# Kernel tuning notes

Measured on AMD Instinct MI355X. Metric: run time of the kernel, lower is better.

Reference implementation:

```python
import jax, jax.numpy as jnp
import numpy as np
from itertools import combinations

NUM_ENT = 7
DIM_ENT = 256
REL_HIDDEN = 256
HIDDEN = 1024
BATCH = 16384
PAIRS = np.array(list(combinations(range(NUM_ENT), 2)), dtype=np.int32)  # [21, 2]


def setup_inputs() -> dict:
    key = jax.random.key(0)
    k1, k2, k3 = jax.random.split(key, 3)
    ctx = jax.random.normal(k1, (BATCH, NUM_ENT * DIM_ENT), dtype=jnp.float32)
    # torch init: uniform(-init_range, init_range) weights, zero bias
    W_rel = jax.random.uniform(k2, (2 * DIM_ENT, REL_HIDDEN), dtype=jnp.float32, minval=-0.01, maxval=0.01)
    b_rel = jnp.zeros((REL_HIDDEN,), dtype=jnp.float32)
    W_fc = jax.random.uniform(k3, (NUM_ENT * DIM_ENT + REL_HIDDEN, HIDDEN), dtype=jnp.float32, minval=-0.01, maxval=0.01)
    b_fc = jnp.zeros((HIDDEN,), dtype=jnp.float32)
    return {"ctx": ctx, "W_rel": W_rel, "b_rel": b_rel, "W_fc": W_fc, "b_fc": b_fc}


def reference(ctx, W_rel, b_rel, W_fc, b_fc):
    B = ctx.shape[0]
    ents = ctx.reshape(B, NUM_ENT, DIM_ENT)
    idx_i = jnp.asarray(PAIRS[:, 0])
    idx_j = jnp.asarray(PAIRS[:, 1])
    # gather both endpoints of each of the 21 pairs: [B, 21, 2*DIM_ENT]
    pair_feat = jnp.concatenate([ents[:, idx_i, :], ents[:, idx_j, :]], axis=-1)
    # batched small Linear + Tanh: [B, 21, REL_HIDDEN]
    rel = jnp.tanh(jnp.einsum("bpe,eh->bph", pair_feat, W_rel) + b_rel)
    # faithful replication of torch: cat pair-major then view(B, rel_hidden, -1).sum(2)
    rel = rel.reshape(B, 21 * REL_HIDDEN).reshape(B, REL_HIDDEN, 21).sum(axis=2)
    inpt = jnp.concatenate([ctx, rel], axis=1)  # [B, input_size]
    # dropout output is discarded in the original forward (no-op); fc1 uses inpt
    out = jnp.tanh(inpt @ W_fc + b_fc)
    return out[None, :, :]  # [1, B, HIDDEN]
```

## Files before the change

kernel.cpp:

```cpp
#include <hip/hip_runtime.h>

typedef unsigned short u16;
typedef unsigned int u32;
typedef __attribute__((ext_vector_type(8))) short short8;
typedef __attribute__((ext_vector_type(4))) float f32x4;
typedef __attribute__((ext_vector_type(2))) u32 u32x2;
typedef const __attribute__((address_space(1))) unsigned int g_u32;
typedef __attribute__((address_space(3))) unsigned int l_u32;

#define BATCH 16384
#define XCOLS 2048

__device__ __forceinline__ void gload16(const void* g, void* l) {
  __builtin_amdgcn_global_load_lds((g_u32*)g, (l_u32*)l, 16, 0, 0);
}
__device__ __forceinline__ u16 f2bf(float f) {
  u32 x = __builtin_bit_cast(u32, f);
  x += 0x7fffu + ((x >> 16) & 1u);
  return (u16)(x >> 16);
}
__device__ __forceinline__ int swz(int P) { return P ^ (((P >> 7) & 7) << 4); }

__device__ __forceinline__ float fast_tanh(float x) {
  float e = __builtin_amdgcn_exp2f(x * 2.885390081777927f);
  return __builtin_fmaf(-2.0f, __builtin_amdgcn_rcpf(e + 1.0f), 1.0f);
}

#define PIPK 0544333222211111000000ULL
#define PJPK 0665654654365432654321ULL

__global__ void prep_ctx(const float* __restrict__ ctx, u16* __restrict__ X) {
  const int total = BATCH * 224;
  for (int u = blockIdx.x * blockDim.x + threadIdx.x; u < total;
       u += gridDim.x * blockDim.x) {
    int b = u / 224, c8 = u - b * 224;
    const float4* s = (const float4*)(ctx + (size_t)b * 1792 + c8 * 8);
    float4 v0 = s[0], v1 = s[1];
    short8 o;
    o[0] = (short)f2bf(v0.x); o[1] = (short)f2bf(v0.y);
    o[2] = (short)f2bf(v0.z); o[3] = (short)f2bf(v0.w);
    o[4] = (short)f2bf(v1.x); o[5] = (short)f2bf(v1.y);
    o[6] = (short)f2bf(v1.z); o[7] = (short)f2bf(v1.w);
    *(short8*)(X + (size_t)b * XCOLS + c8 * 8) = o;
  }
}

__global__ void prep_wrel(const float* __restrict__ Wr, u16* __restrict__ WcT) {
  int idx = blockIdx.x * 256 + threadIdx.x;
  if (idx >= 512 * 256) return;
  int n = idx >> 8, k = idx & 255;
  float v = (n < 256) ? Wr[k * 256 + n] : Wr[(256 + k) * 256 + (n - 256)];
  WcT[idx] = f2bf(v);
}

__global__ void prep_wfc(const float* __restrict__ W, u16* __restrict__ WT) {
  __shared__ float t[64][65];
  int k0 = blockIdx.x * 64;
  int n0 = blockIdx.y * 64;
  int tx = threadIdx.x & 63, ty = threadIdx.x >> 6;
  #pragma unroll
  for (int i = 0; i < 64; i += 4)
    t[ty + i][tx] = W[(size_t)(k0 + ty + i) * 1024 + n0 + tx];
  __syncthreads();
  #pragma unroll
  for (int i = 0; i < 64; i += 4) {
    int n = ty + i;
    WT[(size_t)(n0 + n) * XCOLS + k0 + tx] = f2bf(t[tx][n]);
  }
}

__global__ __launch_bounds__(512, 4) void gemm1_fused(u16* __restrict__ X, const u16* __restrict__ WcT,
                                                      const float* __restrict__ b_rel) {
  __shared__ __align__(16) u16 smem[36864];
  char* sb = (char*)smem;
  const int tid = threadIdx.x;
  const int wid = tid >> 6, lane = tid & 63;
  const int b_base = blockIdx.x * 8;
  f32x4 bias[4] = {};
  if (wid < 4) {
    #pragma unroll
    for (int n = 0; n < 4; ++n)
      bias[n] = *(const f32x4*)(b_rel + wid * 64 + n * 16 + ((lane >> 4) << 2));
  }
  f32x4 acc[4][4] = {};
  for (int kt = 0; kt < 4; ++kt) {
    const int kb = kt * 64;
    {
      int L = swz(tid * 16);
      int row = L >> 7, koff = (L & 127) >> 1;
      int r = row < 56 ? row : 55;
      int bl = r / 7, e = r - bl * 7;
      gload16(X + (size_t)(b_base + bl) * XCOLS + e * 256 + kb + koff, sb + wid * 1024);
    }
    #pragma unroll
    for (int i = 0; i < 8; ++i) {
      int slot = i * 512 + tid;
      int L = swz(slot * 16);
      int rn = L >> 7, koff = (L & 127) >> 1;
      gload16(WcT + rn * 256 + kb + koff, sb + 8192 + (i * 512 + wid * 64) * 16);
    }
    __syncthreads();
    #pragma unroll
    for (int kk = 0; kk < 64; kk += 32) {
      short8 a[4], b[4];
      #pragma unroll
      for (int m = 0; m < 4; ++m) {
        int row = m * 16 + (lane & 15);
        int L = row * 128 + kk * 2 + ((lane >> 4) << 4);
        a[m] = *(const short8*)(sb + swz(L));
      }
      #pragma unroll
      for (int n = 0; n < 4; ++n) {
        int rn = wid * 64 + n * 16 + (lane & 15);
        int L = rn * 128 + kk * 2 + ((lane >> 4) << 4);
        b[n] = *(const short8*)(sb + 8192 + swz(L));
      }
      #pragma unroll
      for (int m = 0; m < 4; ++m)
        #pragma unroll
        for (int n = 0; n < 4; ++n)
          acc[m][n] = __builtin_amdgcn_mfma_f32_16x16x32_bf16(b[n], a[m], acc[m][n], 0, 0, 0);
    }
    __syncthreads();
  }
  float* Tbuf = (float*)(sb + 28672);
  auto stage = [&](int rd) {
    #pragma unroll
    for (int m = 0; m < 4; ++m) {
      int row = m * 16 + (lane & 15);
      int lr = row - rd * 14;
      if (lr >= 0 && lr < 14) {
        #pragma unroll
        for (int n = 0; n < 4; ++n) {
          f32x4 val = acc[m][n] + bias[n];
          int h0 = wid * 64 + n * 16 + ((lane >> 4) << 2);
          int L = lr * 2048 + h0 * 4;
          *(f32x4*)(sb + (L ^ ((lr & 7) << 4))) = val;
        }
      }
    }
  };
  stage(0);
  __syncthreads();
  for (int rd = 0; rd < 4; ++rd) {
    for (int i = tid; i < 2688; i += 512) {
      int bb = i >= 1344;
      int k4 = (i - bb * 1344) << 2;
      int p = k4 >> 8, h0 = k4 & 255;
      int li = bb * 7 + (int)((PIPK >> (3 * p)) & 7);
      int lj = bb * 7 + (int)((PJPK >> (3 * p)) & 7);
      int Lu = (li * 2048 + h0 * 4) ^ ((li & 7) << 4);
      int Lv = (lj * 2048 + 1024 + h0 * 4) ^ ((lj & 7) << 4);
      f32x4 uu = *(const f32x4*)(sb + Lu);
      f32x4 vv = *(const f32x4*)(sb + Lv);
      f32x4 t;
      t[0] = fast_tanh(uu[0] + vv[0]);
      t[1] = fast_tanh(uu[1] + vv[1]);
      t[2] = fast_tanh(uu[2] + vv[2]);
      t[3] = fast_tanh(uu[3] + vv[3]);
      *(f32x4*)(sb + 28672 + (bb * 5376 + k4) * 4) = t;
    }
    __syncthreads();
    {
      int bb = tid >> 8, r = tid & 255;
      const float* T = Tbuf + bb * 5376 + r * 21;
      float s = 0.f;
      #pragma unroll
      for (int c = 0; c < 21; ++c) s += T[c];
      X[(size_t)(b_base + rd * 2 + bb) * XCOLS + 1792 + r] = f2bf(s);
    }
    if (rd < 3) stage(rd + 1);
    __syncthreads();
  }
}

__global__ __launch_bounds__(256, 3) void gemm2(const u16* __restrict__ X, const u16* __restrict__ WT,
                                                const float* __restrict__ b_fc, float* __restrict__ out) {
  __shared__ __align__(16) u16 smem[16384];
  char* sb = (char*)smem;
  const int tid = threadIdx.x;
  const int wid = tid >> 6, lane = tid & 63;
  const int wr = wid >> 1, wc = wid & 1;
  int bid = blockIdx.x;
  int sw = (bid & 7) * 128 + (bid >> 3);
  int bm = sw >> 3, bn = sw & 7;
  const size_t mBase = (size_t)bm * 128;
  const int nBase = bn * 128;
  f32x4 acc[4][4] = {};
  for (int kt = 0; kt < 32; ++kt) {
    const int kb = kt * 64;
    #pragma unroll
    for (int i = 0; i < 4; ++i) {
      int cb = (wid + i * 4) * 64;
      int L = swz((cb + lane) * 16);
      int row = L >> 7, koff = (L & 127) >> 1;
      gload16(X + (mBase + row) * XCOLS + kb + koff, sb + cb * 16);
      gload16(WT + (size_t)(nBase + row) * XCOLS + kb + koff, sb + 16384 + cb * 16);
    }
    __syncthreads();
    #pragma unroll
    for (int kk = 0; kk < 64; kk += 32) {
      short8 a[4], b[4];
      #pragma unroll
      for (int m = 0; m < 4; ++m) {
        int row = wr * 64 + m * 16 + (lane & 15);
        int L = row * 128 + kk * 2 + ((lane >> 4) << 4);
        a[m] = *(const short8*)(sb + swz(L));
      }
      #pragma unroll
      for (int n = 0; n < 4; ++n) {
        int rn = wc * 64 + n * 16 + (lane & 15);
        int L = rn * 128 + kk * 2 + ((lane >> 4) << 4);
        b[n] = *(const short8*)(sb + 16384 + swz(L));
      }
      #pragma unroll
      for (int m = 0; m < 4; ++m)
        #pragma unroll
        for (int n = 0; n < 4; ++n)
          acc[m][n] = __builtin_amdgcn_mfma_f32_16x16x32_bf16(a[m], b[n], acc[m][n], 0, 0, 0);
    }
    __syncthreads();
  }
  #pragma unroll
  for (int m = 0; m < 4; ++m) {
    int row0 = wr * 64 + m * 16 + ((lane >> 4) << 2);
    #pragma unroll
    for (int n = 0; n < 4; ++n) {
      int col = nBase + wc * 64 + n * 16 + (lane & 15);
      float bias = b_fc[col];
      #pragma unroll
      for (int v = 0; v < 4; ++v)
        out[(mBase + row0 + v) * 1024 + col] = fast_tanh(acc[m][n][v] + bias);
    }
  }
}

extern "C" void kernel_launch(void* const* d_in, const int* in_sizes, int n_in,
                              void* d_out, int out_size, void* d_ws, size_t ws_size,
                              hipStream_t stream) {
  const float* ctx   = (const float*)d_in[0];
  const float* W_rel = (const float*)d_in[1];
  const float* b_rel = (const float*)d_in[2];
  const float* W_fc  = (const float*)d_in[3];
  const float* b_fc  = (const float*)d_in[4];
  float* out = (float*)d_out;
  u16* X    = (u16*)d_ws;
  u16* WcT  = X + (size_t)BATCH * XCOLS;
  u16* WfcT = WcT + 512 * 256;
  prep_ctx<<<2048, 256, 0, stream>>>(ctx, X);
  prep_wrel<<<512, 256, 0, stream>>>(W_rel, WcT);
  prep_wfc<<<dim3(32, 16), 256, 0, stream>>>(W_fc, WfcT);
  gemm1_fused<<<2048, 512, 0, stream>>>(X, WcT, b_rel);
  gemm2<<<1024, 256, 0, stream>>>(X, WfcT, b_fc, out);
}
```

Baseline: 201.7 us.

## Triple-buffer gemm2 with 256x128 tiles and fuse pair-tanh reduction in gemm1

```diff
diff --git a/kernel.cpp b/kernel.cpp
--- a/kernel.cpp
+++ b/kernel.cpp
@@ -4,7 +4,6 @@
 typedef unsigned int u32;
 typedef __attribute__((ext_vector_type(8))) short short8;
 typedef __attribute__((ext_vector_type(4))) float f32x4;
-typedef __attribute__((ext_vector_type(2))) u32 u32x2;
 typedef const __attribute__((address_space(1))) unsigned int g_u32;
 typedef __attribute__((address_space(3))) unsigned int l_u32;
 
@@ -123,7 +122,6 @@
     }
     __syncthreads();
   }
-  float* Tbuf = (float*)(sb + 28672);
   auto stage = [&](int rd) {
     #pragma unroll
     for (int m = 0; m < 4; ++m) {
@@ -133,100 +131,130 @@
         #pragma unroll
         for (int n = 0; n < 4; ++n) {
           f32x4 val = acc[m][n] + bias[n];
-          int h0 = wid * 64 + n * 16 + ((lane >> 4) << 2);
-          int L = lr * 2048 + h0 * 4;
+          int h0c = wid * 64 + n * 16 + ((lane >> 4) << 2);
+          int L = lr * 2048 + h0c * 4;
           *(f32x4*)(sb + (L ^ ((lr & 7) << 4))) = val;
         }
       }
     }
   };
   stage(0);
+  const int bb = tid >> 8;
+  const int r = tid & 255;
+  const int R21 = r * 21;
+  const int p0 = R21 >> 8;
+  const int h0 = R21 & 255;
+  const int cx = 256 - h0;
+  const int p1 = p0 < 20 ? p0 + 1 : 20;
+  const int li0 = bb * 7 + (int)((PIPK >> (3 * p0)) & 7);
+  const int lj0 = bb * 7 + (int)((PJPK >> (3 * p0)) & 7);
+  const int li1 = bb * 7 + (int)((PIPK >> (3 * p1)) & 7);
+  const int lj1 = bb * 7 + (int)((PJPK >> (3 * p1)) & 7);
+  const int bU0 = li0 * 2048 + h0 * 4, sU0 = (li0 & 7) << 4;
+  const int bV0 = lj0 * 2048 + 1024 + h0 * 4, sV0 = (lj0 & 7) << 4;
+  const int bU1 = li1 * 2048 - cx * 4, sU1 = (li1 & 7) << 4;
+  const int bV1 = lj1 * 2048 + 1024 - cx * 4, sV1 = (lj1 & 7) << 4;
   __syncthreads();
   for (int rd = 0; rd < 4; ++rd) {
-    for (int i = tid; i < 2688; i += 512) {
-      int bb = i >= 1344;
-      int k4 = (i - bb * 1344) << 2;
-      int p = k4 >> 8, h0 = k4 & 255;
-      int li = bb * 7 + (int)((PIPK >> (3 * p)) & 7);
-      int lj = bb * 7 + (int)((PJPK >> (3 * p)) & 7);
-      int Lu = (li * 2048 + h0 * 4) ^ ((li & 7) << 4);
-      int Lv = (lj * 2048 + 1024 + h0 * 4) ^ ((lj & 7) << 4);
-      f32x4 uu = *(const f32x4*)(sb + Lu);
-      f32x4 vv = *(const f32x4*)(sb + Lv);
-      f32x4 t;
-      t[0] = fast_tanh(uu[0] + vv[0]);
-      t[1] = fast_tanh(uu[1] + vv[1]);
-      t[2] = fast_tanh(uu[2] + vv[2]);
-      t[3] = fast_tanh(uu[3] + vv[3]);
-      *(f32x4*)(sb + 28672 + (bb * 5376 + k4) * 4) = t;
-    }
+    float s = 0.f;
+    #pragma unroll
+    for (int c = 0; c < 21; ++c) {
+      bool sg = c >= cx;
+      int aU = ((sg ? bU1 : bU0) + 4 * c) ^ (sg ? sU1 : sU0);
+      int aV = ((sg ? bV1 : bV0) + 4 * c) ^ (sg ? sV1 : sV0);
+      float u = *(const float*)(sb + aU);
+      float v = *(const float*)(sb + aV);
+      s += fast_tanh(u + v);
+    }
+    X[(size_t)(b_base + rd * 2 + bb) * XCOLS + 1792 + r] = f2bf(s);
     __syncthreads();
-    {
-      int bb = tid >> 8, r = tid & 255;
-      const float* T = Tbuf + bb * 5376 + r * 21;
-      float s = 0.f;
-      #pragma unroll
-      for (int c = 0; c < 21; ++c) s += T[c];
-      X[(size_t)(b_base + rd * 2 + bb) * XCOLS + 1792 + r] = f2bf(s);
-    }
-    if (rd < 3) stage(rd + 1);
-    __syncthreads();
-  }
-}
-
-__global__ __launch_bounds__(256, 3) void gemm2(const u16* __restrict__ X, const u16* __restrict__ WT,
+    if (rd < 3) {
+      stage(rd + 1);
+      __syncthreads();
+    }
+  }
+}
+
+#define G2_BUF 49152
+__global__ __launch_bounds__(512, 2) void gemm2(const u16* __restrict__ X, const u16* __restrict__ WT,
                                                 const float* __restrict__ b_fc, float* __restrict__ out) {
-  __shared__ __align__(16) u16 smem[16384];
+  __shared__ __align__(16) u16 smem[73728];
   char* sb = (char*)smem;
   const int tid = threadIdx.x;
   const int wid = tid >> 6, lane = tid & 63;
-  const int wr = wid >> 1, wc = wid & 1;
+  const int wr = wid >> 2, wc = wid & 3;
   int bid = blockIdx.x;
-  int sw = (bid & 7) * 128 + (bid >> 3);
+  int sw = (bid & 7) * 64 + (bid >> 3);
   int bm = sw >> 3, bn = sw & 7;
-  const size_t mBase = (size_t)bm * 128;
+  const size_t mBase = (size_t)bm * 256;
   const int nBase = bn * 128;
-  f32x4 acc[4][4] = {};
-  for (int kt = 0; kt < 32; ++kt) {
-    const int kb = kt * 64;
+  f32x4 acc[8][2] = {};
+  auto stage2 = [&](int t, int q) {
+    char* Ab = sb + q * G2_BUF;
+    char* Bb = Ab + 32768;
+    const int kb = t * 64;
     #pragma unroll
     for (int i = 0; i < 4; ++i) {
-      int cb = (wid + i * 4) * 64;
-      int L = swz((cb + lane) * 16);
+      int L = swz((i * 512 + tid) * 16);
       int row = L >> 7, koff = (L & 127) >> 1;
-      gload16(X + (mBase + row) * XCOLS + kb + koff, sb + cb * 16);
-      gload16(WT + (size_t)(nBase + row) * XCOLS + kb + koff, sb + 16384 + cb * 16);
-    }
-    __syncthreads();
+      gload16(X + (mBase + row) * XCOLS + kb + koff, Ab + (i * 512 + wid * 64) * 16);
+    }
+    #pragma unroll
+    for (int i = 0; i < 2; ++i) {
+      int L = swz((i * 512 + tid) * 16);
+      int row = L >> 7, koff = (L & 127) >> 1;
+      gload16(WT + (size_t)(nBase + row) * XCOLS + kb + koff, Bb + (i * 512 + wid * 64) * 16);
+    }
+  };
+  auto compute = [&](int q) {
+    char* Ab = sb + q * G2_BUF;
+    char* Bb = Ab + 32768;
     #pragma unroll
     for (int kk = 0; kk < 64; kk += 32) {
-      short8 a[4], b[4];
-      #pragma unroll
-      for (int m = 0; m < 4; ++m) {
-        int row = wr * 64 + m * 16 + (lane & 15);
+      short8 a[8], b[2];
+      #pragma unroll
+      for (int m = 0; m < 8; ++m) {
+        int row = wr * 128 + m * 16 + (lane & 15);
         int L = row * 128 + kk * 2 + ((lane >> 4) << 4);
-        a[m] = *(const short8*)(sb + swz(L));
-      }
-      #pragma unroll
-      for (int n = 0; n < 4; ++n) {
-        int rn = wc * 64 + n * 16 + (lane & 15);
+        a[m] = *(const short8*)(Ab + swz(L));
+      }
+      #pragma unroll
+      for (int n = 0; n < 2; ++n) {
+        int rn = wc * 32 + n * 16 + (lane & 15);
         int L = rn * 128 + kk * 2 + ((lane >> 4) << 4);
-        b[n] = *(const short8*)(sb + 16384 + swz(L));
-      }
-      #pragma unroll
-      for (int m = 0; m < 4; ++m)
+        b[n] = *(const short8*)(Bb + swz(L));
+      }
+      __builtin_amdgcn_s_setprio(1);
+      #pragma unroll
+      for (int m = 0; m < 8; ++m)
         #pragma unroll
-        for (int n = 0; n < 4; ++n)
+        for (int n = 0; n < 2; ++n)
           acc[m][n] = __builtin_amdgcn_mfma_f32_16x16x32_bf16(a[m], b[n], acc[m][n], 0, 0, 0);
-    }
-    __syncthreads();
-  }
+      __builtin_amdgcn_s_setprio(0);
+    }
+  };
+  stage2(0, 0);
+  stage2(1, 1);
+  int qc = 0;
+  for (int t = 0; t < 31; ++t) {
+    asm volatile("s_waitcnt vmcnt(6)" ::: "memory");
+    __builtin_amdgcn_s_barrier();
+    if (t < 30) {
+      int qs = qc + 2 >= 3 ? qc - 1 : qc + 2;
+      stage2(t + 2, qs);
+    }
+    compute(qc);
+    qc = qc + 1 >= 3 ? 0 : qc + 1;
+  }
+  asm volatile("s_waitcnt vmcnt(0)" ::: "memory");
+  __builtin_amdgcn_s_barrier();
+  compute(qc);
   #pragma unroll
-  for (int m = 0; m < 4; ++m) {
-    int row0 = wr * 64 + m * 16 + ((lane >> 4) << 2);
-    #pragma unroll
-    for (int n = 0; n < 4; ++n) {
-      int col = nBase + wc * 64 + n * 16 + (lane & 15);
+  for (int m = 0; m < 8; ++m) {
+    int row0 = wr * 128 + m * 16 + ((lane >> 4) << 2);
+    #pragma unroll
+    for (int n = 0; n < 2; ++n) {
+      int col = nBase + wc * 32 + n * 16 + (lane & 15);
       float bias = b_fc[col];
       #pragma unroll
       for (int v = 0; v < 4; ++v)
@@ -251,5 +279,5 @@
   prep_wrel<<<512, 256, 0, stream>>>(W_rel, WcT);
   prep_wfc<<<dim3(32, 16), 256, 0, stream>>>(W_fc, WfcT);
   gemm1_fused<<<2048, 512, 0, stream>>>(X, WcT, b_rel);
-  gemm2<<<1024, 256, 0, stream>>>(X, WfcT, b_fc, out);
-}
+  gemm2<<<512, 512, 0, stream>>>(X, WfcT, b_fc, out);
+}
```

Result: slower. 206.7 us (+2.5%).
